# Kernel tuning notes

Hardware: AMD Instinct MI355X
Metric: run time of the kernel (lower is better)

Reference implementation:

```python
import jax, jax.numpy as jnp
import numpy as np

N = 100000
D = 128
E = 1600000
NEG_SLOPE = 0.2


def gatv2_layer(x, src, dst, Wl, Wr, att, b):
    # GATv2Conv (heads=1, eval mode): lin_l -> source/message feats, lin_r -> target feats
    xl = x @ Wl                      # [N, D]
    xr = x @ Wr                      # [N, D]
    # per-edge score: a^T LeakyReLU(x_l[src] + x_r[dst])
    z = jax.nn.leaky_relu(xl[src] + xr[dst], NEG_SLOPE)  # [E, D]
    e = z @ att                      # [E]
    # segment softmax over incoming edges of each dst node
    m = jax.ops.segment_max(e, dst, num_segments=N)      # [N]
    ex = jnp.exp(e - m[dst])
    s = jax.ops.segment_sum(ex, dst, num_segments=N)     # [N]
    alpha = ex / (s[dst] + 1e-16)                        # [E]
    # weighted scatter-aggregate of source messages
    out = jax.ops.segment_sum(alpha[:, None] * xl[src], dst, num_segments=N)
    return out + b


def setup_inputs() -> dict:
    key = jax.random.key(0)
    ks = jax.random.split(key, 6)
    scale = 1.0 / np.sqrt(D)
    x = jax.random.normal(ks[0], (N, D), dtype=jnp.float32)
    edge_index = jax.random.randint(ks[1], (2, E), 0, N, dtype=jnp.int64)
    Wl = jax.random.normal(ks[2], (3, D, D), dtype=jnp.float32) * scale
    Wr = jax.random.normal(ks[3], (3, D, D), dtype=jnp.float32) * scale
    att = jax.random.normal(ks[4], (3, D), dtype=jnp.float32) * scale
    b = jax.random.normal(ks[5], (3, D), dtype=jnp.float32) * 0.01
    return {"x": x, "Wl": Wl, "Wr": Wr, "att": att, "b": b, "edge_index": edge_index}


def reference(x, Wl, Wr, att, b, edge_index):
    src, dst = edge_index[0], edge_index[1]
    h = gatv2_layer(x, src, dst, Wl[0], Wr[0], att[0], b[0])
    h = jax.nn.relu(h)
    h = gatv2_layer(h, src, dst, Wl[1], Wr[1], att[1], b[1])
    h = jax.nn.relu(h)
    h = gatv2_layer(h, src, dst, Wl[2], Wr[2], att[2], b[2])
    return h
```

## Files before the change

kernel.cpp:

```cpp
#include <hip/hip_runtime.h>
#include <math.h>

#define DD 128
#define NEG 0.2f

typedef short short8 __attribute__((ext_vector_type(8)));
typedef float f32x4 __attribute__((ext_vector_type(4)));
typedef float f32x2 __attribute__((ext_vector_type(2)));
typedef _Float16 h2v __attribute__((ext_vector_type(2)));

__device__ __forceinline__ unsigned short f2bf(float f) {
    unsigned u = __float_as_uint(f);
    return (unsigned short)((u + 0x7fffu + ((u >> 16) & 1u)) >> 16);
}
__device__ __forceinline__ float bf2f(unsigned short h) {
    return __uint_as_float(((unsigned)h) << 16);
}

__device__ void excl_scan_1024(int* sh, int* aux) {
    __syncthreads();
    int t = threadIdx.x;
    int base = t * 4;
    int a0 = sh[base], a1 = sh[base + 1], a2 = sh[base + 2], a3 = sh[base + 3];
    int s = a0 + a1 + a2 + a3;
    aux[t] = s;
    __syncthreads();
    for (int off = 1; off < 256; off <<= 1) {
        int v = (t >= off) ? aux[t - off] : 0;
        __syncthreads();
        aux[t] += v;
        __syncthreads();
    }
    int excl = aux[t] - s;
    sh[base] = excl;
    sh[base + 1] = excl + a0;
    sh[base + 2] = excl + a0 + a1;
    sh[base + 3] = excl + a0 + a1 + a2;
    __syncthreads();
}

__global__ __launch_bounds__(256) void k_histC(const int* __restrict__ dst,
                                               int* __restrict__ histC, int E, int CB) {
    __shared__ int h[1024];
    int t = threadIdx.x;
    for (int j = t; j < 1024; j += 256) h[j] = 0;
    __syncthreads();
    int stride = gridDim.x * 256;
    for (int i = blockIdx.x * 256 + t; i < E; i += stride)
        atomicAdd(&h[dst[i] >> 7], 1);
    __syncthreads();
    for (int j = t; j < CB; j += 256)
        if (h[j]) atomicAdd(&histC[j], h[j]);
}

__global__ __launch_bounds__(256) void k_scanC2(const int* __restrict__ histC,
                                                int* __restrict__ baseC,
                                                int* __restrict__ cursorC, int CB) {
    __shared__ int sh[1024];
    __shared__ int aux[256];
    int t = threadIdx.x;
    for (int j = t; j < 1024; j += 256) sh[j] = (j < CB) ? histC[j] : 0;
    excl_scan_1024(sh, aux);
    for (int j = t; j <= CB; j += 256) {
        baseC[j] = sh[j];
        if (j < CB) cursorC[j] = sh[j];
    }
}

#define CHUNK 8192
__global__ __launch_bounds__(256) void k_part3(const int* __restrict__ srcI,
                                               const int* __restrict__ dstI,
                                               int* __restrict__ cursorC,
                                               uint2* __restrict__ part,
                                               int E, int CB) {
    __shared__ int sh[1024];
    __shared__ int aux[256];
    __shared__ int resBase[1024];
    __shared__ int cur[1024];
    __shared__ uint2 stage[CHUNK];
    int t = threadIdx.x;
    int c0 = blockIdx.x * CHUNK;
    int cnt = E - c0; if (cnt > CHUNK) cnt = CHUNK;

    for (int j = t; j < 1024; j += 256) sh[j] = 0;
    __syncthreads();
    for (int i = t; i < cnt; i += 256)
        atomicAdd(&sh[dstI[c0 + i] >> 7], 1);
    __syncthreads();
    for (int j = t; j < CB; j += 256) {
        int c = sh[j];
        resBase[j] = c ? atomicAdd(&cursorC[j], c) : 0;
    }
    excl_scan_1024(sh, aux);
    for (int j = t; j < 1024; j += 256) cur[j] = sh[j];
    __syncthreads();
    for (int i = t; i < cnt; i += 256) {
        unsigned s = (unsigned)srcI[c0 + i];
        unsigned d = (unsigned)dstI[c0 + i];
        int b = (int)(d >> 7);
        int pos = atomicAdd(&cur[b], 1);
        stage[pos].x = s;
        stage[pos].y = d;
    }
    __syncthreads();
    for (int i = t; i < cnt; i += 256) {
        uint2 v = stage[i];
        int b = (int)(v.y >> 7);
        part[resBase[b] + (i - sh[b])] = v;
    }
}

__global__ __launch_bounds__(256) void k_part4(const uint2* __restrict__ part,
                                               const int* __restrict__ baseC,
                                               int* __restrict__ srcs,
                                               int* __restrict__ row_ptr,
                                               int N) {
    __shared__ int hist[128];
    __shared__ int incl[128];
    __shared__ int cur[128];
    __shared__ unsigned srcS[8192];
    int b = blockIdx.x;
    int t = threadIdx.x;
    int base = baseC[b];
    int cnt = baseC[b + 1] - base;
    int node0 = b << 7;

    if (t < 128) hist[t] = 0;
    __syncthreads();
    for (int i = t; i < cnt; i += 256)
        atomicAdd(&hist[part[base + i].y & 127], 1);
    __syncthreads();
    if (t < 128) incl[t] = hist[t];
    __syncthreads();
    for (int off = 1; off < 128; off <<= 1) {
        int v = 0;
        if (t < 128 && t >= off) v = incl[t - off];
        __syncthreads();
        if (t < 128) incl[t] += v;
        __syncthreads();
    }
    if (t < 128) cur[t] = incl[t] - hist[t];
    __syncthreads();
    for (int i = t; i < cnt; i += 256) {
        uint2 e = part[base + i];
        int r = atomicAdd(&cur[e.y & 127], 1);
        if (r < 8192) srcS[r] = e.x;
    }
    __syncthreads();
    for (int i = t; i < cnt; i += 256)
        srcs[base + i] = (int)srcS[i];
    int nodes = N - node0; if (nodes > 128) nodes = 128;
    if (t < nodes) row_ptr[node0 + t + 1] = base + incl[t];
    if (b == 0 && t == 0) row_ptr[0] = 0;
}

__global__ void k_castx(const float* __restrict__ x, unsigned short* __restrict__ hi,
                        unsigned short* __restrict__ lo, int n) {
    int i = (blockIdx.x * blockDim.x + threadIdx.x) * 4;
    if (i >= n) return;
    float4 v = *(const float4*)(x + i);
    unsigned short h[4], l[4];
    float f[4] = {v.x, v.y, v.z, v.w};
#pragma unroll
    for (int j = 0; j < 4; j++) {
        h[j] = f2bf(f[j]);
        l[j] = f2bf(f[j] - bf2f(h[j]));
    }
    *(uint2*)(hi + i) = *(uint2*)h;
    *(uint2*)(lo + i) = *(uint2*)l;
}

__global__ void k_castw(const float* __restrict__ Wl, const float* __restrict__ Wr,
                        unsigned short* __restrict__ Wth, unsigned short* __restrict__ Wtl) {
    int idx = blockIdx.x * blockDim.x + threadIdx.x;
    if (idx >= 3 * 256 * 128) return;
    int L = idx >> 15;
    int rem = idx & 32767;
    int nn = rem >> 7;
    int k = rem & 127;
    float v = (nn < 128) ? Wl[L * 16384 + k * 128 + nn]
                         : Wr[L * 16384 + k * 128 + (nn - 128)];
    unsigned short h = f2bf(v);
    Wth[idx] = h;
    Wtl[idx] = f2bf(v - bf2f(h));
}

__global__ __launch_bounds__(256) void k_gemm(const unsigned short* __restrict__ Ahi,
                                              const unsigned short* __restrict__ Alo,
                                              const unsigned short* __restrict__ Wth,
                                              const unsigned short* __restrict__ Wtl,
                                              _Float16* __restrict__ xl, _Float16* __restrict__ xr,
                                              int M, int L) {
    __shared__ unsigned short sA[2][128][40];
    __shared__ unsigned short sB[2][128][40];
    int t = threadIdx.x;
    int lane = t & 63;
    int l15 = lane & 15;
    int quad = lane >> 4;
    int wave = t >> 6;
    int wm = wave & 1;
    int wn = wave >> 1;
    int r0 = blockIdx.x * 128;
    const unsigned short* WthL = Wth + ((size_t)L * 256 + blockIdx.y * 128) * 128;
    const unsigned short* WtlL = Wtl + ((size_t)L * 256 + blockIdx.y * 128) * 128;

    f32x4 acc[4][4] = {};

    for (int kc = 0; kc < 4; kc++) {
        int k0 = kc * 32;
        if (kc) __syncthreads();
#pragma unroll
        for (int i = 0; i < 2; i++) {
            int s = t + i * 256;
            int row = s >> 2;
            int kq = (s & 3) * 8;
            int gr = r0 + row; gr = gr < M ? gr : M - 1;
            uint2 va0 = *(const uint2*)(Ahi + (size_t)gr * DD + k0 + kq);
            uint2 va1 = *(const uint2*)(Ahi + (size_t)gr * DD + k0 + kq + 4);
            *(uint2*)&sA[0][row][kq] = va0;
            *(uint2*)&sA[0][row][kq + 4] = va1;
            uint2 vb0 = *(const uint2*)(Alo + (size_t)gr * DD + k0 + kq);
            uint2 vb1 = *(const uint2*)(Alo + (size_t)gr * DD + k0 + kq + 4);
            *(uint2*)&sA[1][row][kq] = vb0;
            *(uint2*)&sA[1][row][kq + 4] = vb1;
            uint2 wa0 = *(const uint2*)(WthL + (size_t)row * DD + k0 + kq);
            uint2 wa1 = *(const uint2*)(WthL + (size_t)row * DD + k0 + kq + 4);
            *(uint2*)&sB[0][row][kq] = wa0;
            *(uint2*)&sB[0][row][kq + 4] = wa1;
            uint2 wb0 = *(const uint2*)(WtlL + (size_t)row * DD + k0 + kq);
            uint2 wb1 = *(const uint2*)(WtlL + (size_t)row * DD + k0 + kq + 4);
            *(uint2*)&sB[1][row][kq] = wb0;
            *(uint2*)&sB[1][row][kq + 4] = wb1;
        }
        __syncthreads();

        union F8 { short8 v; uint2 u[2]; };
        F8 ah[4], al[4], bh[4], bl[4];
#pragma unroll
        for (int mt = 0; mt < 4; mt++) {
            const unsigned short* p = &sA[0][wm * 64 + mt * 16 + l15][quad * 8];
            ah[mt].u[0] = *(const uint2*)p; ah[mt].u[1] = *(const uint2*)(p + 4);
            const unsigned short* q = &sA[1][wm * 64 + mt * 16 + l15][quad * 8];
            al[mt].u[0] = *(const uint2*)q; al[mt].u[1] = *(const uint2*)(q + 4);
        }
#pragma unroll
        for (int nt = 0; nt < 4; nt++) {
            const unsigned short* p = &sB[0][wn * 64 + nt * 16 + l15][quad * 8];
            bh[nt].u[0] = *(const uint2*)p; bh[nt].u[1] = *(const uint2*)(p + 4);
            const unsigned short* q = &sB[1][wn * 64 + nt * 16 + l15][quad * 8];
            bl[nt].u[0] = *(const uint2*)q; bl[nt].u[1] = *(const uint2*)(q + 4);
        }
#pragma unroll
        for (int mt = 0; mt < 4; mt++)
#pragma unroll
            for (int nt = 0; nt < 4; nt++) {
                acc[mt][nt] = __builtin_amdgcn_mfma_f32_16x16x32_bf16(ah[mt].v, bh[nt].v, acc[mt][nt], 0, 0, 0);
                acc[mt][nt] = __builtin_amdgcn_mfma_f32_16x16x32_bf16(al[mt].v, bh[nt].v, acc[mt][nt], 0, 0, 0);
                acc[mt][nt] = __builtin_amdgcn_mfma_f32_16x16x32_bf16(ah[mt].v, bl[nt].v, acc[mt][nt], 0, 0, 0);
            }
    }

    _Float16* C = blockIdx.y ? xr : xl;
#pragma unroll
    for (int mt = 0; mt < 4; mt++)
#pragma unroll
        for (int r = 0; r < 4; r++) {
            int row = r0 + wm * 64 + mt * 16 + quad * 4 + r;
            if (row < M) {
#pragma unroll
                for (int nt = 0; nt < 4; nt++)
                    C[(size_t)row * DD + wn * 64 + nt * 16 + l15] = (_Float16)acc[mt][nt][r];
            }
        }
}

__global__ __launch_bounds__(256) void k_attn(const _Float16* __restrict__ xl,
                                              const _Float16* __restrict__ xr,
                                              const int* __restrict__ row_ptr,
                                              const int* __restrict__ srcs,
                                              const float* __restrict__ att,
                                              const float* __restrict__ bias,
                                              float* __restrict__ outF,
                                              unsigned short* __restrict__ outHi,
                                              unsigned short* __restrict__ outLo,
                                              int n, int mode) {
    int gtid = blockIdx.x * blockDim.x + threadIdx.x;
    int d = gtid >> 4;
    if (d >= n) return;
    int l = threadIdx.x & 15;

    union Q { uint4 q; h2v h[4]; };

    h2v at[4], xrh[4];
    {
        float4 a0 = *(const float4*)(att + l * 8);
        float4 a1 = *(const float4*)(att + l * 8 + 4);
        at[0] = h2v{(_Float16)a0.x, (_Float16)a0.y};
        at[1] = h2v{(_Float16)a0.z, (_Float16)a0.w};
        at[2] = h2v{(_Float16)a1.x, (_Float16)a1.y};
        at[3] = h2v{(_Float16)a1.z, (_Float16)a1.w};
        Q hr; hr.q = *(const uint4*)(xr + (size_t)d * DD + l * 8);
#pragma unroll
        for (int j = 0; j < 4; j++) xrh[j] = hr.h[j];
    }
    const _Float16 cneg = (_Float16)NEG;

    int beg = row_ptr[d], end = row_ptr[d + 1];
    float lse = 0.f;
    f32x2 av[4] = {};

    for (int i = beg; i < end; i++) {
        int s = srcs[i];
        Q hx; hx.q = *(const uint4*)(xl + (size_t)s * DD + l * 8);
        float p = 0.f;
#pragma unroll
        for (int j = 0; j < 4; j++) {
            h2v z = hx.h[j] + xrh[j];
            h2v zl = __builtin_elementwise_max(z, z * cneg);
            p = __builtin_amdgcn_fdot2(zl, at[j], p, false);
        }
        p += __shfl_xor(p, 1, 64);
        p += __shfl_xor(p, 2, 64);
        p += __shfl_xor(p, 4, 64);
        p += __shfl_xor(p, 8, 64);
        p = fminf(fmaxf(p, -60.f), 60.f);
        float w = __expf(p);
        lse += w;
#pragma unroll
        for (int j = 0; j < 4; j++) {
            f32x2 xv = {(float)hx.h[j][0], (float)hx.h[j][1]};
            av[j] += xv * w;
        }
    }
    float inv = (end > beg) ? 1.0f / lse : 0.f;
    float o[8];
    {
        float4 b0 = *(const float4*)(bias + l * 8);
        float4 b1 = *(const float4*)(bias + l * 8 + 4);
        float bv[8] = {b0.x, b0.y, b0.z, b0.w, b1.x, b1.y, b1.z, b1.w};
#pragma unroll
        for (int j = 0; j < 4; j++) {
            o[2 * j]     = av[j][0] * inv + bv[2 * j];
            o[2 * j + 1] = av[j][1] * inv + bv[2 * j + 1];
        }
    }
    if (mode) {
        union U8 { unsigned short s[8]; uint4 q; };
        U8 hh, ll;
#pragma unroll
        for (int j = 0; j < 8; j++) {
            float v = fmaxf(o[j], 0.f);
            hh.s[j] = f2bf(v);
            ll.s[j] = f2bf(v - bf2f(hh.s[j]));
        }
        *(uint4*)(outHi + (size_t)d * DD + l * 8) = hh.q;
        *(uint4*)(outLo + (size_t)d * DD + l * 8) = ll.q;
    } else {
        float4 o0 = {o[0], o[1], o[2], o[3]};
        float4 o1 = {o[4], o[5], o[6], o[7]};
        float* op = outF + (size_t)d * DD + l * 8;
        *(float4*)op = o0;
        *(float4*)(op + 4) = o1;
    }
}

extern "C" void kernel_launch(void* const* d_in, const int* in_sizes, int n_in,
                              void* d_out, int out_size, void* d_ws, size_t ws_size,
                              hipStream_t stream) {
    const float* x    = (const float*)d_in[0];
    const float* Wl   = (const float*)d_in[1];
    const float* Wr   = (const float*)d_in[2];
    const float* att  = (const float*)d_in[3];
    const float* bias = (const float*)d_in[4];
    const int*   ei   = (const int*)d_in[5];

    int N = in_sizes[0] / DD;
    int E = in_sizes[5] / 2;
    const int* srcI = ei;
    const int* dstI = ei + E;
    float* out = (float*)d_out;
    int CB = (N + 127) >> 7;

    char* ws = (char*)d_ws;
    size_t off = 0;
    auto alloc = [&](size_t bytes) -> void* {
        void* p = ws + off;
        off += (bytes + 255) & ~(size_t)255;
        return p;
    };
    _Float16*       xl   = (_Float16*)alloc((size_t)N * DD * 2);
    _Float16*       xr   = (_Float16*)alloc((size_t)N * DD * 2);
    unsigned short* Ahi  = (unsigned short*)alloc((size_t)N * DD * 2);
    unsigned short* Alo  = (unsigned short*)alloc((size_t)N * DD * 2);
    unsigned short* Wth  = (unsigned short*)alloc((size_t)3 * 256 * 128 * 2);
    unsigned short* Wtl  = (unsigned short*)alloc((size_t)3 * 256 * 128 * 2);
    uint2* part    = (uint2*)alloc((size_t)E * 8);
    int*   srcs    = (int*)alloc((size_t)E * 4);
    int*   row_ptr = (int*)alloc((size_t)(N + 1) * 4);
    int*   histC   = (int*)alloc((size_t)(CB + 1) * 4);
    int*   baseC   = (int*)alloc((size_t)(CB + 1) * 4);
    int*   cursorC = (int*)alloc((size_t)(CB + 1) * 4);

    const int tb = 256;
    (void)hipMemsetAsync(histC, 0, (size_t)CB * 4, stream);
    k_histC<<<256, 256, 0, stream>>>(dstI, histC, E, CB);
    k_scanC2<<<1, 256, 0, stream>>>(histC, baseC, cursorC, CB);
    k_part3<<<(E + CHUNK - 1) / CHUNK, 256, 0, stream>>>(srcI, dstI, cursorC, part, E, CB);
    k_part4<<<CB, 256, 0, stream>>>(part, baseC, srcs, row_ptr, N);

    k_castw<<<(3 * 256 * 128 + tb - 1) / tb, tb, 0, stream>>>(Wl, Wr, Wth, Wtl);
    k_castx<<<((size_t)N * DD / 4 + tb - 1) / tb, tb, 0, stream>>>(x, Ahi, Alo, N * DD);

    int gX = (N + 127) / 128;
    for (int L = 0; L < 3; ++L) {
        k_gemm<<<dim3(gX, 2), 256, 0, stream>>>(Ahi, Alo, Wth, Wtl, xl, xr, N, L);
        k_attn<<<((size_t)N * 16 + tb - 1) / tb, tb, 0, stream>>>(
            xl, xr, row_ptr, srcs, att + (size_t)L * DD, bias + (size_t)L * DD,
            out, Ahi, Alo, N, (L < 2) ? 1 : 0);
    }
}
```

Before: 530.1 us.

## Process each destination node with a full wavefront and eight edges in flight

The attention kernel now gives each destination node a 64-lane wavefront split into four 16-lane groups, each handling two edges per iteration. Source indices for the next iteration are prefetched, and partial sums are combined across groups with cross-lane shuffles before one group writes the output. The softmax exponent now uses exp2 with attention weights pre-scaled by log2(e). This exposes more memory-level parallelism for the gathered rows, at the cost of four times as many threads, idle lanes on low-degree nodes, and extra reduction shuffles.

```diff
diff --git a/kernel.cpp b/kernel.cpp
--- a/kernel.cpp
+++ b/kernel.cpp
@@ -16,6 +16,12 @@
 __device__ __forceinline__ float bf2f(unsigned short h) {
     return __uint_as_float(((unsigned)h) << 16);
 }
+
+#if __has_builtin(__builtin_amdgcn_exp2f)
+#define EXP2F(x) __builtin_amdgcn_exp2f(x)
+#else
+#define EXP2F(x) exp2f(x)
+#endif
 
 __device__ void excl_scan_1024(int* sh, int* aux) {
     __syncthreads();
@@ -284,22 +290,24 @@
                                               unsigned short* __restrict__ outHi,
                                               unsigned short* __restrict__ outLo,
                                               int n, int mode) {
-    int gtid = blockIdx.x * blockDim.x + threadIdx.x;
-    int d = gtid >> 4;
+    int d = (blockIdx.x * blockDim.x + threadIdx.x) >> 6;
     if (d >= n) return;
-    int l = threadIdx.x & 15;
+    int l = threadIdx.x & 63;
+    int l15 = l & 15;
+    int g = l >> 4;
 
     union Q { uint4 q; h2v h[4]; };
+    const float LOG2E = 1.44269504088896f;
 
     h2v at[4], xrh[4];
     {
-        float4 a0 = *(const float4*)(att + l * 8);
-        float4 a1 = *(const float4*)(att + l * 8 + 4);
-        at[0] = h2v{(_Float16)a0.x, (_Float16)a0.y};
-        at[1] = h2v{(_Float16)a0.z, (_Float16)a0.w};
-        at[2] = h2v{(_Float16)a1.x, (_Float16)a1.y};
-        at[3] = h2v{(_Float16)a1.z, (_Float16)a1.w};
-        Q hr; hr.q = *(const uint4*)(xr + (size_t)d * DD + l * 8);
+        float4 a0 = *(const float4*)(att + l15 * 8);
+        float4 a1 = *(const float4*)(att + l15 * 8 + 4);
+        at[0] = h2v{(_Float16)(a0.x * LOG2E), (_Float16)(a0.y * LOG2E)};
+        at[1] = h2v{(_Float16)(a0.z * LOG2E), (_Float16)(a0.w * LOG2E)};
+        at[2] = h2v{(_Float16)(a1.x * LOG2E), (_Float16)(a1.y * LOG2E)};
+        at[3] = h2v{(_Float16)(a1.z * LOG2E), (_Float16)(a1.w * LOG2E)};
+        Q hr; hr.q = *(const uint4*)(xr + (size_t)d * DD + l15 * 8);
 #pragma unroll
         for (int j = 0; j < 4; j++) xrh[j] = hr.h[j];
     }
@@ -307,60 +315,87 @@
 
     int beg = row_ptr[d], end = row_ptr[d + 1];
     float lse = 0.f;
-    f32x2 av[4] = {};
-
-    for (int i = beg; i < end; i++) {
-        int s = srcs[i];
-        Q hx; hx.q = *(const uint4*)(xl + (size_t)s * DD + l * 8);
-        float p = 0.f;
+    float av[8] = {};
+
+    int i0 = beg + g, i1 = beg + 4 + g;
+    bool v0 = i0 < end, v1 = i1 < end;
+    int s0 = (end > beg) ? srcs[v0 ? i0 : beg] : 0;
+    int s1 = (end > beg) ? srcs[v1 ? i1 : beg] : 0;
+
+    const _Float16* xlp = xl + l15 * 8;
+
+    for (int i = beg; i < end; i += 8) {
+        Q h0, h1;
+        h0.q = *(const uint4*)(xlp + (size_t)s0 * DD);
+        h1.q = *(const uint4*)(xlp + (size_t)s1 * DD);
+        int n0 = i + 8 + g, n1 = i + 12 + g;
+        bool nv0 = n0 < end, nv1 = n1 < end;
+        int t0 = srcs[nv0 ? n0 : beg];
+        int t1 = srcs[nv1 ? n1 : beg];
+
+        float p0 = 0.f, p1 = 0.f;
 #pragma unroll
         for (int j = 0; j < 4; j++) {
-            h2v z = hx.h[j] + xrh[j];
-            h2v zl = __builtin_elementwise_max(z, z * cneg);
-            p = __builtin_amdgcn_fdot2(zl, at[j], p, false);
-        }
-        p += __shfl_xor(p, 1, 64);
-        p += __shfl_xor(p, 2, 64);
-        p += __shfl_xor(p, 4, 64);
-        p += __shfl_xor(p, 8, 64);
-        p = fminf(fmaxf(p, -60.f), 60.f);
-        float w = __expf(p);
-        lse += w;
+            h2v z0 = h0.h[j] + xrh[j];
+            h2v zl0 = __builtin_elementwise_max(z0, z0 * cneg);
+            p0 = __builtin_amdgcn_fdot2(zl0, at[j], p0, false);
+            h2v z1 = h1.h[j] + xrh[j];
+            h2v zl1 = __builtin_elementwise_max(z1, z1 * cneg);
+            p1 = __builtin_amdgcn_fdot2(zl1, at[j], p1, false);
+        }
+        p0 += __shfl_xor(p0, 1, 64);  p1 += __shfl_xor(p1, 1, 64);
+        p0 += __shfl_xor(p0, 2, 64);  p1 += __shfl_xor(p1, 2, 64);
+        p0 += __shfl_xor(p0, 4, 64);  p1 += __shfl_xor(p1, 4, 64);
+        p0 += __shfl_xor(p0, 8, 64);  p1 += __shfl_xor(p1, 8, 64);
+        p0 = fminf(fmaxf(p0, -86.f), 86.f);
+        p1 = fminf(fmaxf(p1, -86.f), 86.f);
+        float w0 = v0 ? EXP2F(p0) : 0.f;
+        float w1 = v1 ? EXP2F(p1) : 0.f;
+        lse += w0 + w1;
 #pragma unroll
         for (int j = 0; j < 4; j++) {
-            f32x2 xv = {(float)hx.h[j][0], (float)hx.h[j][1]};
-            av[j] += xv * w;
-        }
-    }
-    float inv = (end > beg) ? 1.0f / lse : 0.f;
-    float o[8];
-    {
-        float4 b0 = *(const float4*)(bias + l * 8);
-        float4 b1 = *(const float4*)(bias + l * 8 + 4);
+            av[2 * j]     += (float)h0.h[j][0] * w0;
+            av[2 * j + 1] += (float)h0.h[j][1] * w0;
+            av[2 * j]     += (float)h1.h[j][0] * w1;
+            av[2 * j + 1] += (float)h1.h[j][1] * w1;
+        }
+        s0 = t0; s1 = t1; v0 = nv0; v1 = nv1;
+    }
+
+    lse += __shfl_xor(lse, 16, 64);
+    lse += __shfl_xor(lse, 32, 64);
+#pragma unroll
+    for (int j = 0; j < 8; j++) {
+        av[j] += __shfl_xor(av[j], 16, 64);
+        av[j] += __shfl_xor(av[j], 32, 64);
+    }
+
+    if (l < 16) {
+        float inv = (end > beg) ? 1.0f / lse : 0.f;
+        float o[8];
+        float4 b0 = *(const float4*)(bias + l15 * 8);
+        float4 b1 = *(const float4*)(bias + l15 * 8 + 4);
         float bv[8] = {b0.x, b0.y, b0.z, b0.w, b1.x, b1.y, b1.z, b1.w};
 #pragma unroll
-        for (int j = 0; j < 4; j++) {
-            o[2 * j]     = av[j][0] * inv + bv[2 * j];
-            o[2 * j + 1] = av[j][1] * inv + bv[2 * j + 1];
-        }
-    }
-    if (mode) {
-        union U8 { unsigned short s[8]; uint4 q; };
-        U8 hh, ll;
-#pragma unroll
-        for (int j = 0; j < 8; j++) {
-            float v = fmaxf(o[j], 0.f);
-            hh.s[j] = f2bf(v);
-            ll.s[j] = f2bf(v - bf2f(hh.s[j]));
-        }
-        *(uint4*)(outHi + (size_t)d * DD + l * 8) = hh.q;
-        *(uint4*)(outLo + (size_t)d * DD + l * 8) = ll.q;
-    } else {
-        float4 o0 = {o[0], o[1], o[2], o[3]};
-        float4 o1 = {o[4], o[5], o[6], o[7]};
-        float* op = outF + (size_t)d * DD + l * 8;
-        *(float4*)op = o0;
-        *(float4*)(op + 4) = o1;
+        for (int j = 0; j < 8; j++) o[j] = av[j] * inv + bv[j];
+        if (mode) {
+            union U8 { unsigned short s[8]; uint4 q; };
+            U8 hh, ll;
+#pragma unroll
+            for (int j = 0; j < 8; j++) {
+                float v = fmaxf(o[j], 0.f);
+                hh.s[j] = f2bf(v);
+                ll.s[j] = f2bf(v - bf2f(hh.s[j]));
+            }
+            *(uint4*)(outHi + (size_t)d * DD + l15 * 8) = hh.q;
+            *(uint4*)(outLo + (size_t)d * DD + l15 * 8) = ll.q;
+        } else {
+            float4 o0 = {o[0], o[1], o[2], o[3]};
+            float4 o1 = {o[4], o[5], o[6], o[7]};
+            float* op = outF + (size_t)d * DD + l15 * 8;
+            *(float4*)op = o0;
+            *(float4*)(op + 4) = o1;
+        }
     }
 }
 
@@ -414,7 +449,7 @@
     int gX = (N + 127) / 128;
     for (int L = 0; L < 3; ++L) {
         k_gemm<<<dim3(gX, 2), 256, 0, stream>>>(Ahi, Alo, Wth, Wtl, xl, xr, N, L);
-        k_attn<<<((size_t)N * 16 + tb - 1) / tb, tb, 0, stream>>>(
+        k_attn<<<((size_t)N * 64 + tb - 1) / tb, tb, 0, stream>>>(
             xl, xr, row_ptr, srcs, att + (size_t)L * DD, bias + (size_t)L * DD,
             out, Ahi, Alo, N, (L < 2) ? 1 : 0);
     }
```

Result: faster. 515.4 us (-2.8%).
